# Kernel tuning notes

Hardware: AMD Instinct MI355X
Metric: run time of the kernel (lower is better)

The kernel has to match this reference:

```python
import jax, jax.numpy as jnp
import numpy as np

N = 100000   # nodes
E = 1600000  # edges
D = 64       # in_dim == hidden
H = 64       # hidden
L = 5        # GIN layers
G = 128      # graphs in batch
OUT = 10     # out_dim
BN_EPS = 1e-5


def setup_inputs() -> dict:
    key = jax.random.key(0)
    ks = jax.random.split(key, 16)
    x = jax.random.normal(ks[0], (N, D), dtype=jnp.float32)
    ei = jax.random.randint(ks[1], (2, E), 0, N, dtype=jnp.int64)
    b = jnp.sort(jax.random.randint(ks[2], (N,), 0, G, dtype=jnp.int64))
    s = 0.1
    return {
        "x": x,
        "ei": ei,
        "b": b,
        "conv_W1": jax.random.normal(ks[3], (L, D, H), dtype=jnp.float32) * s,
        "conv_b1": jnp.zeros((L, H), dtype=jnp.float32),
        "conv_W2": jax.random.normal(ks[4], (L, H, H), dtype=jnp.float32) * s,
        "conv_b2": jnp.zeros((L, H), dtype=jnp.float32),
        "bn_gamma": jnp.ones((L, H), dtype=jnp.float32),
        "bn_beta": jnp.zeros((L, H), dtype=jnp.float32),
        "head_W1": jax.random.normal(ks[5], (H, H), dtype=jnp.float32) * s,
        "head_b1": jnp.zeros((H,), dtype=jnp.float32),
        "head_W2": jax.random.normal(ks[6], (H, OUT), dtype=jnp.float32) * s,
        "head_b2": jnp.zeros((OUT,), dtype=jnp.float32),
    }


def reference(x, ei, b, conv_W1, conv_b1, conv_W2, conv_b2,
              bn_gamma, bn_beta, head_W1, head_b1, head_W2, head_b2):
    src, dst = ei[0], ei[1]
    for l in range(L):
        # GINConv (eps=0): h = x + sum_{j in N(i)} x_j  via gather + scatter-add
        agg = jax.ops.segment_sum(x[src], dst, num_segments=N)  # [N, d]
        h = x + agg
        # nn MLP: Linear -> ReLU -> Linear
        h = jax.nn.relu(h @ conv_W1[l] + conv_b1[l]) @ conv_W2[l] + conv_b2[l]
        # BatchNorm over node dim (batch statistics), then ReLU (dropout: eval)
        mean = jnp.mean(h, axis=0)
        var = jnp.var(h, axis=0)
        h = bn_gamma[l] * (h - mean) * jax.lax.rsqrt(var + BN_EPS) + bn_beta[l]
        x = jax.nn.relu(h)
    # global mean pool per graph
    sums = jax.ops.segment_sum(x, b, num_segments=G)                 # [G, H]
    cnts = jax.ops.segment_sum(jnp.ones((N,), x.dtype), b, num_segments=G)
    pooled = sums / jnp.maximum(cnts, 1.0)[:, None]
    # head: Linear -> ReLU -> (Dropout eval) -> Linear
    return jax.nn.relu(pooled @ head_W1 + head_b1) @ head_W2 + head_b2
```

## Files before the change

### kernel.cpp

```cpp
#include <hip/hip_runtime.h>

#define N_NODES 100000
#define N_EDGES 1600000
#define HDIM    64
#define NLAYERS 5
#define NGRAPH  128
#define NOUT    10
#define BN_EPS  1e-5f
#define NBUCK   196
#define EPB     8192


__global__ __launch_bounds__(256) void k_hist(const int* __restrict__ dst, int* __restrict__ counts) {
    int e = blockIdx.x * 256 + threadIdx.x;
    if (e < N_EDGES) atomicAdd(&counts[dst[e]], 1);
}

__global__ __launch_bounds__(256) void k_scan_bt(const int* __restrict__ counts, int* __restrict__ bsums) {
    __shared__ int sm[256];
    int t = threadIdx.x;
    int base = blockIdx.x * 1024 + t * 4;
    int s = 0;
#pragma unroll
    for (int k = 0; k < 4; ++k) { int i = base + k; s += (i < N_NODES) ? counts[i] : 0; }
    sm[t] = s; __syncthreads();
    for (int o = 128; o > 0; o >>= 1) { if (t < o) sm[t] += sm[t + o]; __syncthreads(); }
    if (t == 0) bsums[blockIdx.x] = sm[0];
}

__global__ void k_scan_tot(int* bsums, int nblk, int* offsets) {
    if (threadIdx.x == 0 && blockIdx.x == 0) {
        int run = 0;
        for (int i = 0; i < nblk; ++i) { int v = bsums[i]; bsums[i] = run; run += v; }
        offsets[N_NODES] = N_EDGES;
    }
}

__global__ __launch_bounds__(256) void k_scan_fin(const int* __restrict__ counts, const int* __restrict__ bsums,
                                                 int* __restrict__ offsets, int* __restrict__ cursor) {
    __shared__ int sm[256];
    int t = threadIdx.x;
    int base = blockIdx.x * 1024 + t * 4;
    int v[4]; int s = 0;
#pragma unroll
    for (int k = 0; k < 4; ++k) { int i = base + k; v[k] = (i < N_NODES) ? counts[i] : 0; s += v[k]; }
    sm[t] = s; __syncthreads();
    for (int o = 1; o < 256; o <<= 1) {
        int add = (t >= o) ? sm[t - o] : 0;
        __syncthreads();
        sm[t] += add;
        __syncthreads();
    }
    int run = bsums[blockIdx.x] + (sm[t] - s);
#pragma unroll
    for (int k = 0; k < 4; ++k) {
        int i = base + k;
        if (i < N_NODES) { offsets[i] = run; cursor[i] = run; run += v[k]; }
    }
}

__global__ void k_binit(const int* __restrict__ offs, int* __restrict__ bcursor) {
    int b = blockIdx.x * 256 + threadIdx.x;
    if (b < NBUCK) bcursor[b] = offs[b << 9];
}

__global__ __launch_bounds__(1024) void k_binfill(const int* __restrict__ src, const int* __restrict__ dst,
                                                  int* __restrict__ bcursor, unsigned* __restrict__ tmp) {
    __shared__ unsigned slots[EPB];
    __shared__ int cnt[NBUCK], lcur[NBUCK], gbase[NBUCK];
    __shared__ int lbase[NBUCK + 1];
    __shared__ int sscan[256];
    int t = threadIdx.x;
    int e0 = blockIdx.x * EPB;
    for (int i = t; i < NBUCK; i += 1024) { cnt[i] = 0; lcur[i] = 0; }
    __syncthreads();
    unsigned pk[8]; int bk[8];
#pragma unroll
    for (int k = 0; k < 8; ++k) {
        int e = e0 + k * 1024 + t;
        bk[k] = -1;
        if (e < N_EDGES) {
            int s = src[e], d = dst[e];
            int b = d >> 9;
            pk[k] = ((unsigned)(d & 511) << 17) | (unsigned)s;
            bk[k] = b;
            atomicAdd(&cnt[b], 1);
        }
    }
    __syncthreads();
    if (t < 256) sscan[t] = (t < NBUCK) ? cnt[t] : 0;
    __syncthreads();
    for (int o = 1; o < 256; o <<= 1) {
        int v = 0;
        if (t < 256 && t >= o) v = sscan[t - o];
        __syncthreads();
        if (t < 256) sscan[t] += v;
        __syncthreads();
    }
    if (t < NBUCK) {
        lbase[t] = sscan[t] - cnt[t];
        gbase[t] = atomicAdd(&bcursor[t], cnt[t]);
    }
    if (t == 0) lbase[NBUCK] = sscan[255];
    __syncthreads();
#pragma unroll
    for (int k = 0; k < 8; ++k) {
        if (bk[k] >= 0) {
            int pos = lbase[bk[k]] + atomicAdd(&lcur[bk[k]], 1);
            slots[pos] = pk[k];
        }
    }
    __syncthreads();
    int total = lbase[NBUCK];
    for (int i = t; i < total; i += 1024) {
        int lo = 0, hi = NBUCK - 1;
        while (lo < hi) { int mid = (lo + hi + 1) >> 1; if (lbase[mid] <= i) lo = mid; else hi = mid - 1; }
        tmp[gbase[lo] + (i - lbase[lo])] = slots[i];
    }
}

__global__ __launch_bounds__(1024) void k_localcsr(const unsigned* __restrict__ tmp, const int* __restrict__ offs,
                                                   int* __restrict__ cursor, int* __restrict__ csr) {
    int b = blockIdx.x;
    int nlo = b << 9;
    int nhi = nlo + 512; if (nhi > N_NODES) nhi = N_NODES;
    int base = offs[nlo], end = offs[nhi];
    for (int i = base + (int)threadIdx.x; i < end; i += 1024) {
        unsigned pk = tmp[i];
        int node = nlo + (int)(pk >> 17);
        int p = atomicAdd(&cursor[node], 1);
        csr[p] = (int)(pk & 0x1FFFFu);
    }
}


static __device__ __forceinline__ void bn_coeffs(const float* stats, const float* gam, const float* bet,
                                                 int j0, float4& sc, float4& sh) {
    const float invN = 1.0f / (float)N_NODES;
    float m, v, s;
    m = stats[j0+0]*invN; v = stats[64+j0+0]*invN - m*m; s = gam[j0+0]*rsqrtf(v+BN_EPS); sc.x = s; sh.x = bet[j0+0]-m*s;
    m = stats[j0+1]*invN; v = stats[64+j0+1]*invN - m*m; s = gam[j0+1]*rsqrtf(v+BN_EPS); sc.y = s; sh.y = bet[j0+1]-m*s;
    m = stats[j0+2]*invN; v = stats[64+j0+2]*invN - m*m; s = gam[j0+2]*rsqrtf(v+BN_EPS); sc.z = s; sh.z = bet[j0+2]-m*s;
    m = stats[j0+3]*invN; v = stats[64+j0+3]*invN - m*m; s = gam[j0+3]*rsqrtf(v+BN_EPS); sc.w = s; sh.w = bet[j0+3]-m*s;
}

static __device__ __forceinline__ float4 bn_apply(float4 v, const float4& sc, const float4& sh) {
    v.x = fmaxf(fmaf(v.x, sc.x, sh.x), 0.f);
    v.y = fmaxf(fmaf(v.y, sc.y, sh.y), 0.f);
    v.z = fmaxf(fmaf(v.z, sc.z, sh.z), 0.f);
    v.w = fmaxf(fmaf(v.w, sc.w, sh.w), 0.f);
    return v;
}

template <bool APPLY>
__global__ __launch_bounds__(256) void k_agg(const float4* __restrict__ x4, const int* __restrict__ offsets,
                                             const int* __restrict__ csr, float4* __restrict__ agg4,
                                             const float* __restrict__ stats, const float* __restrict__ gam,
                                             const float* __restrict__ bet) {
    int tid = blockIdx.x * 256 + threadIdx.x;
    int n = tid >> 4, q = tid & 15;
    if (n >= N_NODES) return;
    float4 sc, sh;
    if (APPLY) bn_coeffs(stats, gam, bet, q * 4, sc, sh);
    int beg = offsets[n], end = offsets[n + 1];
    float4 a0 = make_float4(0.f, 0.f, 0.f, 0.f);
    float4 a1 = make_float4(0.f, 0.f, 0.f, 0.f);
    int e = beg;
    for (; e + 1 < end; e += 2) {
        int s0 = csr[e], s1 = csr[e + 1];
        float4 v0 = x4[(size_t)s0 * 16 + q];
        float4 v1 = x4[(size_t)s1 * 16 + q];
        if (APPLY) { v0 = bn_apply(v0, sc, sh); v1 = bn_apply(v1, sc, sh); }
        a0.x += v0.x; a0.y += v0.y; a0.z += v0.z; a0.w += v0.w;
        a1.x += v1.x; a1.y += v1.y; a1.z += v1.z; a1.w += v1.w;
    }
    if (e < end) {
        int s0 = csr[e];
        float4 v0 = x4[(size_t)s0 * 16 + q];
        if (APPLY) v0 = bn_apply(v0, sc, sh);
        a0.x += v0.x; a0.y += v0.y; a0.z += v0.z; a0.w += v0.w;
    }
    a0.x += a1.x; a0.y += a1.y; a0.z += a1.z; a0.w += a1.w;
    agg4[(size_t)n * 16 + q] = a0;
}

#define MLP_TB 128
#define ROWS   68
template <bool APPLY>
__global__ __launch_bounds__(MLP_TB) void k_mlp2(const float* __restrict__ x, float* __restrict__ aggh2,
                                                 const float* __restrict__ W1, const float* __restrict__ b1,
                                                 const float* __restrict__ W2, const float* __restrict__ b2,
                                                 const float* __restrict__ statsPrev, const float* __restrict__ gam,
                                                 const float* __restrict__ bet, float* __restrict__ statsOut) {
    __shared__ float sm[MLP_TB * ROWS];
    __shared__ float red1[MLP_TB], red2[MLP_TB];
    int t = threadIdx.x;
    int base = blockIdx.x * MLP_TB;
    {
        int q = t & 15;
        float4 sc, sh;
        if (APPLY) bn_coeffs(statsPrev, gam, bet, q * 4, sc, sh);
        for (int i = t; i < MLP_TB * 16; i += MLP_TB) {
            int r = i >> 4;
            int n = base + r; if (n >= N_NODES) n = N_NODES - 1;
            float4 xv = ((const float4*)x)[(size_t)n * 16 + q];
            if (APPLY) xv = bn_apply(xv, sc, sh);
            float4 av = ((const float4*)aggh2)[(size_t)n * 16 + q];
            float4 s; s.x = xv.x + av.x; s.y = xv.y + av.y; s.z = xv.z + av.z; s.w = xv.w + av.w;
            *((float4*)&sm[r * ROWS + q * 4]) = s;
        }
    }
    __syncthreads();
    int n = base + t;
    bool valid = n < N_NODES;
    float* row = &sm[t * ROWS];
    float acc[64];
#pragma unroll
    for (int j = 0; j < 64; ++j) acc[j] = b1[j];
    for (int k = 0; k < 64; ++k) {
        float xk = row[k];
        const float* w = &W1[k * 64];
#pragma unroll
        for (int j = 0; j < 64; ++j) acc[j] = fmaf(xk, w[j], acc[j]);
    }
#pragma unroll
    for (int q = 0; q < 16; ++q) {
        float4 h;
        h.x = fmaxf(acc[4 * q + 0], 0.f);
        h.y = fmaxf(acc[4 * q + 1], 0.f);
        h.z = fmaxf(acc[4 * q + 2], 0.f);
        h.w = fmaxf(acc[4 * q + 3], 0.f);
        *((float4*)&row[q * 4]) = h;
    }
#pragma unroll
    for (int j = 0; j < 64; ++j) acc[j] = b2[j];
    for (int k = 0; k < 64; ++k) {
        float xk = row[k];
        const float* w = &W2[k * 64];
#pragma unroll
        for (int j = 0; j < 64; ++j) acc[j] = fmaf(xk, w[j], acc[j]);
    }
    if (valid) {
        float4* o = (float4*)(aggh2 + (size_t)n * 64);
#pragma unroll
        for (int q = 0; q < 16; ++q)
            o[q] = make_float4(acc[4 * q + 0], acc[4 * q + 1], acc[4 * q + 2], acc[4 * q + 3]);
    }
#pragma unroll
    for (int q = 0; q < 16; ++q) {
        float4 h;
        if (valid) h = make_float4(acc[4*q+0], acc[4*q+1], acc[4*q+2], acc[4*q+3]);
        else       h = make_float4(0.f, 0.f, 0.f, 0.f);
        *((float4*)&row[q * 4]) = h;
    }
    __syncthreads();
    {
        int j = t & 63, half = t >> 6;
        float s = 0.f, sq = 0.f;
        const float* col = &sm[(half * 64) * ROWS + j];
#pragma unroll 8
        for (int r = 0; r < 64; ++r) { float v = col[r * ROWS]; s += v; sq += v * v; }
        red1[t] = s; red2[t] = sq;
    }
    __syncthreads();
    if (t < 64) {
        atomicAdd(&statsOut[t], red1[t] + red1[t + 64]);
    } else {
        int j = t - 64;
        atomicAdd(&statsOut[64 + j], red2[j] + red2[j + 64]);
    }
}


__global__ void k_bounds(const int* __restrict__ b, int* __restrict__ bounds) {
    int g = threadIdx.x;
    if (g > NGRAPH) return;
    int lo = 0, hi = N_NODES;
    while (lo < hi) { int mid = (lo + hi) >> 1; if (b[mid] < g) lo = mid + 1; else hi = mid; }
    bounds[g] = lo;
}

__global__ __launch_bounds__(256) void k_pool(const float4* __restrict__ x4, const int* __restrict__ bounds,
                                              float4* __restrict__ pooled4, const float* __restrict__ stats,
                                              const float* __restrict__ gam, const float* __restrict__ bet) {
    int g = blockIdx.x;
    int beg = bounds[g], end = bounds[g + 1];
    int t = threadIdx.x;
    int q = t & 15;
    int w = t >> 4;
    float4 sc, sh;
    bn_coeffs(stats, gam, bet, q * 4, sc, sh);
    float4 a = make_float4(0.f, 0.f, 0.f, 0.f);
    for (int n = beg + w; n < end; n += 16) {
        float4 v = bn_apply(x4[(size_t)n * 16 + q], sc, sh);
        a.x += v.x; a.y += v.y; a.z += v.z; a.w += v.w;
    }
    __shared__ float4 sm[16][16];
    sm[w][q] = a; __syncthreads();
    for (int o = 8; o > 0; o >>= 1) {
        if (w < o) {
            float4 u = sm[w + o][q];
            sm[w][q].x += u.x; sm[w][q].y += u.y; sm[w][q].z += u.z; sm[w][q].w += u.w;
        }
        __syncthreads();
    }
    if (w == 0) {
        float inv = (end > beg) ? 1.0f / (float)(end - beg) : 0.0f;
        float4 r = sm[0][q];
        r.x *= inv; r.y *= inv; r.z *= inv; r.w *= inv;
        pooled4[g * 16 + q] = r;
    }
}

__global__ __launch_bounds__(128) void k_head(const float* __restrict__ pooled,
                                              const float* __restrict__ W1, const float* __restrict__ b1,
                                              const float* __restrict__ W2, const float* __restrict__ b2,
                                              float* __restrict__ out) {
    __shared__ float w1s[64 * 64];
    __shared__ float w2s[64 * NOUT];
    int t = threadIdx.x;
    for (int i = t; i < 64 * 64; i += 128) w1s[i] = W1[i];
    for (int i = t; i < 64 * NOUT; i += 128) w2s[i] = W2[i];
    __syncthreads();
    int g = t;
    float pr[64];
#pragma unroll
    for (int k = 0; k < 64; ++k) pr[k] = pooled[g * 64 + k];
    float acc[NOUT];
#pragma unroll
    for (int o = 0; o < NOUT; ++o) acc[o] = b2[o];
    for (int j = 0; j < 64; ++j) {
        float h = b1[j];
#pragma unroll
        for (int k = 0; k < 64; ++k) h = fmaf(pr[k], w1s[k * 64 + j], h);
        h = fmaxf(h, 0.f);
#pragma unroll
        for (int o = 0; o < NOUT; ++o) acc[o] = fmaf(h, w2s[j * NOUT + o], acc[o]);
    }
#pragma unroll
    for (int o = 0; o < NOUT; ++o) out[g * NOUT + o] = acc[o];
}


extern "C" void kernel_launch(void* const* d_in, const int* in_sizes, int n_in,
                              void* d_out, int out_size, void* d_ws, size_t ws_size,
                              hipStream_t stream) {
    const float* x0  = (const float*)d_in[0];
    const int*   ei  = (const int*)d_in[1];
    const int*   b   = (const int*)d_in[2];
    const float* cW1 = (const float*)d_in[3];
    const float* cb1 = (const float*)d_in[4];
    const float* cW2 = (const float*)d_in[5];
    const float* cb2 = (const float*)d_in[6];
    const float* gam = (const float*)d_in[7];
    const float* bet = (const float*)d_in[8];
    const float* hW1 = (const float*)d_in[9];
    const float* hb1 = (const float*)d_in[10];
    const float* hW2 = (const float*)d_in[11];
    const float* hb2 = (const float*)d_in[12];
    float* out = (float*)d_out;

    char* ws = (char*)d_ws;
    size_t off = 0;
    auto alloc = [&](size_t bytes) { void* p = ws + off; off += (bytes + 255) & ~(size_t)255; return p; };
    float* bufA   = (float*)alloc((size_t)N_NODES * 64 * sizeof(float));
    float* bufB   = (float*)alloc((size_t)N_NODES * 64 * sizeof(float));
    int*   csr    = (int*)alloc((size_t)N_EDGES * sizeof(int));
    int*   counts = (int*)alloc((size_t)(N_NODES + 1) * sizeof(int));
    int*   offs   = (int*)alloc((size_t)(N_NODES + 1) * sizeof(int));
    int*   cursor = (int*)alloc((size_t)(N_NODES + 1) * sizeof(int));
    int*   bsums  = (int*)alloc(256 * sizeof(int));
    int*   bcursor= (int*)alloc(256 * sizeof(int));
    float* stats  = (float*)alloc(NLAYERS * 128 * sizeof(float));
    float* pooled = (float*)alloc(NGRAPH * 64 * sizeof(float));
    int*   bounds = (int*)alloc((NGRAPH + 1) * sizeof(int));
    unsigned* tmp = (unsigned*)bufB;

    const int* src = ei;
    const int* dst = ei + N_EDGES;

    hipMemsetAsync(counts, 0, (N_NODES + 1) * sizeof(int), stream);
    hipMemsetAsync(stats, 0, NLAYERS * 128 * sizeof(float), stream);

    const int EB = (N_EDGES + 255) / 256;
    const int SB = (N_NODES + 1023) / 1024;
    const int FB = (N_EDGES + EPB - 1) / EPB;
    k_hist<<<EB, 256, 0, stream>>>(dst, counts);
    k_scan_bt<<<SB, 256, 0, stream>>>(counts, bsums);
    k_scan_tot<<<1, 1, 0, stream>>>(bsums, SB, offs);
    k_scan_fin<<<SB, 256, 0, stream>>>(counts, bsums, offs, cursor);
    k_binit<<<1, 256, 0, stream>>>(offs, bcursor);
    k_binfill<<<FB, 1024, 0, stream>>>(src, dst, bcursor, tmp);
    k_localcsr<<<NBUCK, 1024, 0, stream>>>(tmp, offs, cursor, csr);
    k_bounds<<<1, NGRAPH + 1, 0, stream>>>(b, bounds);

    const int AB = (N_NODES * 16 + 255) / 256;
    const int MB_G = (N_NODES + MLP_TB - 1) / MLP_TB;

    const float* P = x0;
    float* Q = bufA;
    float* spare = bufB;
    for (int l = 0; l < NLAYERS; ++l) {
        const float* sPrev = stats + (size_t)(l - 1) * 128;
        const float* gPrev = gam + (size_t)(l - 1) * 64;
        const float* bPrev = bet + (size_t)(l - 1) * 64;
        if (l == 0) {
            k_agg<false><<<AB, 256, 0, stream>>>((const float4*)P, offs, csr, (float4*)Q,
                                                 nullptr, nullptr, nullptr);
            k_mlp2<false><<<MB_G, MLP_TB, 0, stream>>>(P, Q,
                                                       cW1, cb1, cW2, cb2,
                                                       nullptr, nullptr, nullptr, stats);
        } else {
            k_agg<true><<<AB, 256, 0, stream>>>((const float4*)P, offs, csr, (float4*)Q,
                                                sPrev, gPrev, bPrev);
            k_mlp2<true><<<MB_G, MLP_TB, 0, stream>>>(P, Q,
                                                      cW1 + (size_t)l * 64 * 64, cb1 + l * 64,
                                                      cW2 + (size_t)l * 64 * 64, cb2 + l * 64,
                                                      sPrev, gPrev, bPrev, stats + (size_t)l * 128);
        }
        float* newSpare = (P == x0) ? spare : (float*)P;
        P = Q;
        Q = newSpare;
    }

    k_pool<<<NGRAPH, 256, 0, stream>>>((const float4*)P, bounds, (float4*)pooled,
                                       stats + 4 * 128, gam + 4 * 64, bet + 4 * 64);
    k_head<<<1, 128, 0, stream>>>(pooled, hW1, hb1, hW2, hb2, out);
}
```

Measured before the change: 830.2 us.

## Run GIN MLP on MFMA with split-bf16 (hi/lo) emulated fp32

Replaces the scalar-FMA per-node MLP kernel with a wave-per-16-node-tile kernel that uses bf16 MFMA 16x16x32 instructions. Precision is kept by a three-term hi/lo split of operands. A prologue kernel pre-converts the weights into the MFMA B-fragment layout, and the grid becomes persistent with register accumulation of the BN statistics. This trades the 64-register fp32 accumulator loop for matrix-core throughput, at the cost of extra conversion work and slightly different rounding.

```diff
diff --git a/kernel.cpp b/kernel.cpp
--- a/kernel.cpp
+++ b/kernel.cpp
@@ -9,6 +9,19 @@
 #define BN_EPS  1e-5f
 #define NBUCK   196
 #define EPB     8192
+#define NTILES  (N_NODES / 16)
+
+typedef __attribute__((ext_vector_type(8))) short bf16x8;
+typedef __attribute__((ext_vector_type(4))) float f32x4;
+
+static __device__ __forceinline__ unsigned short f2bf(float f) {
+    unsigned u = __float_as_uint(f);
+    unsigned r = (u + 0x7FFFu + ((u >> 16) & 1u)) >> 16;
+    return (unsigned short)r;
+}
+static __device__ __forceinline__ float bf2f(unsigned short h) {
+    return __uint_as_float(((unsigned)h) << 16);
+}
 
 
 __global__ __launch_bounds__(256) void k_hist(const int* __restrict__ dst, int* __restrict__ counts) {
@@ -130,6 +143,27 @@
         int node = nlo + (int)(pk >> 17);
         int p = atomicAdd(&cursor[node], 1);
         csr[p] = (int)(pk & 0x1FFFFu);
+    }
+}
+
+__global__ __launch_bounds__(256) void k_wcvt(const float* __restrict__ cW1, const float* __restrict__ cW2,
+                                              unsigned short* __restrict__ whi, unsigned short* __restrict__ wlo) {
+    int tid = blockIdx.x * 256 + threadIdx.x;
+    if (tid >= 5120) return;
+    int lane = tid & 63;
+    int r = tid >> 6;
+    int nt = r & 3;
+    int ks = (r >> 2) & 1;
+    int gemm = (r >> 3) & 1;
+    int layer = r >> 4;
+    const float* W = (gemm ? cW2 : cW1) + (size_t)layer * 4096;
+    size_t ob = ((size_t)r * 64 + lane) * 8;
+#pragma unroll
+    for (int j = 0; j < 8; ++j) {
+        float w = W[(32 * ks + 8 * (lane >> 4) + j) * 64 + 16 * nt + (lane & 15)];
+        unsigned short h = f2bf(w);
+        whi[ob + j] = h;
+        wlo[ob + j] = f2bf(w - bf2f(h));
     }
 }
 
@@ -184,90 +218,134 @@
     agg4[(size_t)n * 16 + q] = a0;
 }
 
-#define MLP_TB 128
-#define ROWS   68
 template <bool APPLY>
-__global__ __launch_bounds__(MLP_TB) void k_mlp2(const float* __restrict__ x, float* __restrict__ aggh2,
-                                                 const float* __restrict__ W1, const float* __restrict__ b1,
-                                                 const float* __restrict__ W2, const float* __restrict__ b2,
-                                                 const float* __restrict__ statsPrev, const float* __restrict__ gam,
-                                                 const float* __restrict__ bet, float* __restrict__ statsOut) {
-    __shared__ float sm[MLP_TB * ROWS];
-    __shared__ float red1[MLP_TB], red2[MLP_TB];
+__global__ __launch_bounds__(256) void k_mlp3(const float* __restrict__ x, float* __restrict__ aggh2,
+                                              const unsigned short* __restrict__ w1hi, const unsigned short* __restrict__ w1lo,
+                                              const unsigned short* __restrict__ w2hi, const unsigned short* __restrict__ w2lo,
+                                              const float* __restrict__ b1, const float* __restrict__ b2,
+                                              const float* __restrict__ statsPrev, const float* __restrict__ gam,
+                                              const float* __restrict__ bet, float* __restrict__ statsOut) {
+    __shared__ float h1s[4][16 * 68];
     int t = threadIdx.x;
-    int base = blockIdx.x * MLP_TB;
-    {
-        int q = t & 15;
-        float4 sc, sh;
-        if (APPLY) bn_coeffs(statsPrev, gam, bet, q * 4, sc, sh);
-        for (int i = t; i < MLP_TB * 16; i += MLP_TB) {
-            int r = i >> 4;
-            int n = base + r; if (n >= N_NODES) n = N_NODES - 1;
-            float4 xv = ((const float4*)x)[(size_t)n * 16 + q];
-            if (APPLY) xv = bn_apply(xv, sc, sh);
-            float4 av = ((const float4*)aggh2)[(size_t)n * 16 + q];
-            float4 s; s.x = xv.x + av.x; s.y = xv.y + av.y; s.z = xv.z + av.z; s.w = xv.w + av.w;
-            *((float4*)&sm[r * ROWS + q * 4]) = s;
-        }
-    }
-    __syncthreads();
-    int n = base + t;
-    bool valid = n < N_NODES;
-    float* row = &sm[t * ROWS];
-    float acc[64];
-#pragma unroll
-    for (int j = 0; j < 64; ++j) acc[j] = b1[j];
-    for (int k = 0; k < 64; ++k) {
-        float xk = row[k];
-        const float* w = &W1[k * 64];
-#pragma unroll
-        for (int j = 0; j < 64; ++j) acc[j] = fmaf(xk, w[j], acc[j]);
-    }
-#pragma unroll
-    for (int q = 0; q < 16; ++q) {
-        float4 h;
-        h.x = fmaxf(acc[4 * q + 0], 0.f);
-        h.y = fmaxf(acc[4 * q + 1], 0.f);
-        h.z = fmaxf(acc[4 * q + 2], 0.f);
-        h.w = fmaxf(acc[4 * q + 3], 0.f);
-        *((float4*)&row[q * 4]) = h;
-    }
-#pragma unroll
-    for (int j = 0; j < 64; ++j) acc[j] = b2[j];
-    for (int k = 0; k < 64; ++k) {
-        float xk = row[k];
-        const float* w = &W2[k * 64];
-#pragma unroll
-        for (int j = 0; j < 64; ++j) acc[j] = fmaf(xk, w[j], acc[j]);
-    }
-    if (valid) {
-        float4* o = (float4*)(aggh2 + (size_t)n * 64);
-#pragma unroll
-        for (int q = 0; q < 16; ++q)
-            o[q] = make_float4(acc[4 * q + 0], acc[4 * q + 1], acc[4 * q + 2], acc[4 * q + 3]);
-    }
-#pragma unroll
-    for (int q = 0; q < 16; ++q) {
-        float4 h;
-        if (valid) h = make_float4(acc[4*q+0], acc[4*q+1], acc[4*q+2], acc[4*q+3]);
-        else       h = make_float4(0.f, 0.f, 0.f, 0.f);
-        *((float4*)&row[q * 4]) = h;
-    }
-    __syncthreads();
-    {
-        int j = t & 63, half = t >> 6;
-        float s = 0.f, sq = 0.f;
-        const float* col = &sm[(half * 64) * ROWS + j];
-#pragma unroll 8
-        for (int r = 0; r < 64; ++r) { float v = col[r * ROWS]; s += v; sq += v * v; }
-        red1[t] = s; red2[t] = sq;
-    }
-    __syncthreads();
-    if (t < 64) {
-        atomicAdd(&statsOut[t], red1[t] + red1[t + 64]);
-    } else {
-        int j = t - 64;
-        atomicAdd(&statsOut[64 + j], red2[j] + red2[j + 64]);
+    int lane = t & 63;
+    int wv = t >> 6;
+    int lr = lane & 15;
+    int lg = lane >> 4;
+    int nw = gridDim.x * 4;
+    float* myh1 = &h1s[wv][0];
+
+    float sc[16], sh[16];
+    if (APPLY) {
+        const float invN = 1.0f / (float)N_NODES;
+#pragma unroll
+        for (int ks = 0; ks < 2; ++ks)
+#pragma unroll
+            for (int j = 0; j < 8; ++j) {
+                int f = 32 * ks + 8 * lg + j;
+                float m = statsPrev[f] * invN;
+                float v = statsPrev[64 + f] * invN - m * m;
+                float s = gam[f] * rsqrtf(v + BN_EPS);
+                sc[ks * 8 + j] = s; sh[ks * 8 + j] = bet[f] - m * s;
+            }
+    }
+    float bias1[4], bias2[4];
+#pragma unroll
+    for (int nt = 0; nt < 4; ++nt) { bias1[nt] = b1[16 * nt + lr]; bias2[nt] = b2[16 * nt + lr]; }
+
+    float st_s[4] = {0.f, 0.f, 0.f, 0.f}, st_q[4] = {0.f, 0.f, 0.f, 0.f};
+
+    for (int base = blockIdx.x * 4; base < NTILES; base += nw) {
+        int tile = base + wv;
+        bool act = tile < NTILES;
+        bf16x8 Ah[2], Al[2];
+        f32x4 acc[4];
+        if (act) {
+            int node = tile * 16 + lr;
+#pragma unroll
+            for (int ks = 0; ks < 2; ++ks) {
+                int f0 = 32 * ks + 8 * lg;
+                const float* xr = x + (size_t)node * 64 + f0;
+                const float* ar = aggh2 + (size_t)node * 64 + f0;
+                float4 xv0 = *(const float4*)xr, xv1 = *(const float4*)(xr + 4);
+                float4 av0 = *(const float4*)ar, av1 = *(const float4*)(ar + 4);
+                float in[8] = {xv0.x, xv0.y, xv0.z, xv0.w, xv1.x, xv1.y, xv1.z, xv1.w};
+                float ag[8] = {av0.x, av0.y, av0.z, av0.w, av1.x, av1.y, av1.z, av1.w};
+#pragma unroll
+                for (int j = 0; j < 8; ++j) {
+                    float v = in[j];
+                    if (APPLY) v = fmaxf(fmaf(v, sc[ks * 8 + j], sh[ks * 8 + j]), 0.f);
+                    v += ag[j];
+                    unsigned short h = f2bf(v);
+                    Ah[ks][j] = (short)h;
+                    Al[ks][j] = (short)f2bf(v - bf2f(h));
+                }
+            }
+#pragma unroll
+            for (int nt = 0; nt < 4; ++nt) {
+                f32x4 c = {bias1[nt], bias1[nt], bias1[nt], bias1[nt]};
+#pragma unroll
+                for (int ks = 0; ks < 2; ++ks) {
+                    bf16x8 bh = *(const bf16x8*)(w1hi + ((size_t)((ks * 4 + nt) * 64 + lane)) * 8);
+                    bf16x8 bl = *(const bf16x8*)(w1lo + ((size_t)((ks * 4 + nt) * 64 + lane)) * 8);
+                    c = __builtin_amdgcn_mfma_f32_16x16x32_bf16(Ah[ks], bh, c, 0, 0, 0);
+                    c = __builtin_amdgcn_mfma_f32_16x16x32_bf16(Ah[ks], bl, c, 0, 0, 0);
+                    c = __builtin_amdgcn_mfma_f32_16x16x32_bf16(Al[ks], bh, c, 0, 0, 0);
+                }
+                acc[nt] = c;
+            }
+#pragma unroll
+            for (int nt = 0; nt < 4; ++nt)
+#pragma unroll
+                for (int r = 0; r < 4; ++r)
+                    myh1[(4 * lg + r) * 68 + 16 * nt + lr] = fmaxf(acc[nt][r], 0.f);
+        }
+        __syncthreads();
+        if (act) {
+            bf16x8 A2h[2], A2l[2];
+#pragma unroll
+            for (int ks = 0; ks < 2; ++ks) {
+                const float* hr = &myh1[lr * 68 + 32 * ks + 8 * lg];
+                float4 h0 = *(const float4*)hr;
+                float4 h1v = *(const float4*)(hr + 4);
+                float hv[8] = {h0.x, h0.y, h0.z, h0.w, h1v.x, h1v.y, h1v.z, h1v.w};
+#pragma unroll
+                for (int j = 0; j < 8; ++j) {
+                    unsigned short hh = f2bf(hv[j]);
+                    A2h[ks][j] = (short)hh;
+                    A2l[ks][j] = (short)f2bf(hv[j] - bf2f(hh));
+                }
+            }
+            int nodeb = (base + wv) * 16;
+#pragma unroll
+            for (int nt = 0; nt < 4; ++nt) {
+                f32x4 c = {bias2[nt], bias2[nt], bias2[nt], bias2[nt]};
+#pragma unroll
+                for (int ks = 0; ks < 2; ++ks) {
+                    bf16x8 bh = *(const bf16x8*)(w2hi + ((size_t)((ks * 4 + nt) * 64 + lane)) * 8);
+                    bf16x8 bl = *(const bf16x8*)(w2lo + ((size_t)((ks * 4 + nt) * 64 + lane)) * 8);
+                    c = __builtin_amdgcn_mfma_f32_16x16x32_bf16(A2h[ks], bh, c, 0, 0, 0);
+                    c = __builtin_amdgcn_mfma_f32_16x16x32_bf16(A2h[ks], bl, c, 0, 0, 0);
+                    c = __builtin_amdgcn_mfma_f32_16x16x32_bf16(A2l[ks], bh, c, 0, 0, 0);
+                }
+#pragma unroll
+                for (int r = 0; r < 4; ++r) {
+                    float v = c[r];
+                    aggh2[(size_t)(nodeb + 4 * lg + r) * 64 + 16 * nt + lr] = v;
+                    st_s[nt] += v; st_q[nt] += v * v;
+                }
+            }
+        }
+        __syncthreads();
+    }
+#pragma unroll
+    for (int nt = 0; nt < 4; ++nt) {
+        float s = st_s[nt], q = st_q[nt];
+        s += __shfl_xor(s, 16); q += __shfl_xor(q, 16);
+        s += __shfl_xor(s, 32); q += __shfl_xor(q, 32);
+        if (lg == 0) {
+            atomicAdd(&statsOut[16 * nt + lr], s);
+            atomicAdd(&statsOut[64 + 16 * nt + lr], q);
+        }
     }
 }
 
@@ -374,6 +452,8 @@
     float* stats  = (float*)alloc(NLAYERS * 128 * sizeof(float));
     float* pooled = (float*)alloc(NGRAPH * 64 * sizeof(float));
     int*   bounds = (int*)alloc((NGRAPH + 1) * sizeof(int));
+    unsigned short* whi = (unsigned short*)alloc(5 * 2 * 4096 * sizeof(unsigned short));
+    unsigned short* wlo = (unsigned short*)alloc(5 * 2 * 4096 * sizeof(unsigned short));
     unsigned* tmp = (unsigned*)bufB;
 
     const int* src = ei;
@@ -393,9 +473,10 @@
     k_binfill<<<FB, 1024, 0, stream>>>(src, dst, bcursor, tmp);
     k_localcsr<<<NBUCK, 1024, 0, stream>>>(tmp, offs, cursor, csr);
     k_bounds<<<1, NGRAPH + 1, 0, stream>>>(b, bounds);
+    k_wcvt<<<20, 256, 0, stream>>>(cW1, cW2, whi, wlo);
 
     const int AB = (N_NODES * 16 + 255) / 256;
-    const int MB_G = (N_NODES + MLP_TB - 1) / MLP_TB;
+    const int MG = 782;
 
     const float* P = x0;
     float* Q = bufA;
@@ -404,19 +485,22 @@
         const float* sPrev = stats + (size_t)(l - 1) * 128;
         const float* gPrev = gam + (size_t)(l - 1) * 64;
         const float* bPrev = bet + (size_t)(l - 1) * 64;
+        const unsigned short* w1h = whi + (size_t)(l * 2) * 4096;
+        const unsigned short* w1l = wlo + (size_t)(l * 2) * 4096;
+        const unsigned short* w2h = whi + (size_t)(l * 2 + 1) * 4096;
+        const unsigned short* w2l = wlo + (size_t)(l * 2 + 1) * 4096;
         if (l == 0) {
             k_agg<false><<<AB, 256, 0, stream>>>((const float4*)P, offs, csr, (float4*)Q,
                                                  nullptr, nullptr, nullptr);
-            k_mlp2<false><<<MB_G, MLP_TB, 0, stream>>>(P, Q,
-                                                       cW1, cb1, cW2, cb2,
-                                                       nullptr, nullptr, nullptr, stats);
+            k_mlp3<false><<<MG, 256, 0, stream>>>(P, Q, w1h, w1l, w2h, w2l,
+                                                  cb1, cb2,
+                                                  nullptr, nullptr, nullptr, stats);
         } else {
             k_agg<true><<<AB, 256, 0, stream>>>((const float4*)P, offs, csr, (float4*)Q,
                                                 sPrev, gPrev, bPrev);
-            k_mlp2<true><<<MB_G, MLP_TB, 0, stream>>>(P, Q,
-                                                      cW1 + (size_t)l * 64 * 64, cb1 + l * 64,
-                                                      cW2 + (size_t)l * 64 * 64, cb2 + l * 64,
-                                                      sPrev, gPrev, bPrev, stats + (size_t)l * 128);
+            k_mlp3<true><<<MG, 256, 0, stream>>>(P, Q, w1h, w1l, w2h, w2l,
+                                                 cb1 + l * 64, cb2 + l * 64,
+                                                 sPrev, gPrev, bPrev, stats + (size_t)l * 128);
         }
         float* newSpare = (P == x0) ? spare : (float*)P;
         P = Q;
```

Result: slower. 964.0 us (+16.1%).

## Fold self-term into aggregation and split MLP matmul into column halves

Applied to the files above, without the earlier changes.

The aggregation kernel now seeds its accumulator with the node's own (BN-applied) feature, so the MLP kernel no longer reads x separately or applies the previous batch-norm. This removes one full N×64 read per layer from the MLP kernel. The MLP inner loops are also split into two 32-column halves with an un-unrolled outer loop, meant to lower instruction and register pressure, though each row element is now read from shared memory twice.

```diff
diff --git a/kernel.cpp b/kernel.cpp
--- a/kernel.cpp
+++ b/kernel.cpp
@@ -163,7 +163,8 @@
     float4 sc, sh;
     if (APPLY) bn_coeffs(stats, gam, bet, q * 4, sc, sh);
     int beg = offsets[n], end = offsets[n + 1];
-    float4 a0 = make_float4(0.f, 0.f, 0.f, 0.f);
+    float4 a0 = x4[(size_t)n * 16 + q];
+    if (APPLY) a0 = bn_apply(a0, sc, sh);
     float4 a1 = make_float4(0.f, 0.f, 0.f, 0.f);
     int e = beg;
     for (; e + 1 < end; e += 2) {
@@ -186,29 +187,19 @@
 
 #define MLP_TB 128
 #define ROWS   68
-template <bool APPLY>
-__global__ __launch_bounds__(MLP_TB) void k_mlp2(const float* __restrict__ x, float* __restrict__ aggh2,
+__global__ __launch_bounds__(MLP_TB) void k_mlp6(float* __restrict__ aggh2,
                                                  const float* __restrict__ W1, const float* __restrict__ b1,
                                                  const float* __restrict__ W2, const float* __restrict__ b2,
-                                                 const float* __restrict__ statsPrev, const float* __restrict__ gam,
-                                                 const float* __restrict__ bet, float* __restrict__ statsOut) {
+                                                 float* __restrict__ statsOut) {
     __shared__ float sm[MLP_TB * ROWS];
     __shared__ float red1[MLP_TB], red2[MLP_TB];
     int t = threadIdx.x;
     int base = blockIdx.x * MLP_TB;
-    {
-        int q = t & 15;
-        float4 sc, sh;
-        if (APPLY) bn_coeffs(statsPrev, gam, bet, q * 4, sc, sh);
-        for (int i = t; i < MLP_TB * 16; i += MLP_TB) {
-            int r = i >> 4;
-            int n = base + r; if (n >= N_NODES) n = N_NODES - 1;
-            float4 xv = ((const float4*)x)[(size_t)n * 16 + q];
-            if (APPLY) xv = bn_apply(xv, sc, sh);
-            float4 av = ((const float4*)aggh2)[(size_t)n * 16 + q];
-            float4 s; s.x = xv.x + av.x; s.y = xv.y + av.y; s.z = xv.z + av.z; s.w = xv.w + av.w;
-            *((float4*)&sm[r * ROWS + q * 4]) = s;
-        }
+    for (int i = t; i < MLP_TB * 16; i += MLP_TB) {
+        int r = i >> 4, q = i & 15;
+        int n = base + r; if (n >= N_NODES) n = N_NODES - 1;
+        float4 av = ((const float4*)aggh2)[(size_t)n * 16 + q];
+        *((float4*)&sm[r * ROWS + q * 4]) = av;
     }
     __syncthreads();
     int n = base + t;
@@ -217,11 +208,14 @@
     float acc[64];
 #pragma unroll
     for (int j = 0; j < 64; ++j) acc[j] = b1[j];
-    for (int k = 0; k < 64; ++k) {
-        float xk = row[k];
-        const float* w = &W1[k * 64];
-#pragma unroll
-        for (int j = 0; j < 64; ++j) acc[j] = fmaf(xk, w[j], acc[j]);
+#pragma unroll 1
+    for (int jh = 0; jh < 2; ++jh) {
+        for (int k = 0; k < 64; ++k) {
+            float xk = row[k];
+            const float* w = &W1[k * 64 + jh * 32];
+#pragma unroll
+            for (int j = 0; j < 32; ++j) acc[jh * 32 + j] = fmaf(xk, w[j], acc[jh * 32 + j]);
+        }
     }
 #pragma unroll
     for (int q = 0; q < 16; ++q) {
@@ -234,11 +228,14 @@
     }
 #pragma unroll
     for (int j = 0; j < 64; ++j) acc[j] = b2[j];
-    for (int k = 0; k < 64; ++k) {
-        float xk = row[k];
-        const float* w = &W2[k * 64];
-#pragma unroll
-        for (int j = 0; j < 64; ++j) acc[j] = fmaf(xk, w[j], acc[j]);
+#pragma unroll 1
+    for (int jh = 0; jh < 2; ++jh) {
+        for (int k = 0; k < 64; ++k) {
+            float xk = row[k];
+            const float* w = &W2[k * 64 + jh * 32];
+#pragma unroll
+            for (int j = 0; j < 32; ++j) acc[jh * 32 + j] = fmaf(xk, w[j], acc[jh * 32 + j]);
+        }
     }
     if (valid) {
         float4* o = (float4*)(aggh2 + (size_t)n * 64);
@@ -407,17 +404,14 @@
         if (l == 0) {
             k_agg<false><<<AB, 256, 0, stream>>>((const float4*)P, offs, csr, (float4*)Q,
                                                  nullptr, nullptr, nullptr);
-            k_mlp2<false><<<MB_G, MLP_TB, 0, stream>>>(P, Q,
-                                                       cW1, cb1, cW2, cb2,
-                                                       nullptr, nullptr, nullptr, stats);
         } else {
             k_agg<true><<<AB, 256, 0, stream>>>((const float4*)P, offs, csr, (float4*)Q,
                                                 sPrev, gPrev, bPrev);
-            k_mlp2<true><<<MB_G, MLP_TB, 0, stream>>>(P, Q,
-                                                      cW1 + (size_t)l * 64 * 64, cb1 + l * 64,
-                                                      cW2 + (size_t)l * 64 * 64, cb2 + l * 64,
-                                                      sPrev, gPrev, bPrev, stats + (size_t)l * 128);
-        }
+        }
+        k_mlp6<<<MB_G, MLP_TB, 0, stream>>>(Q,
+                                            cW1 + (size_t)l * 64 * 64, cb1 + l * 64,
+                                            cW2 + (size_t)l * 64 * 64, cb2 + l * 64,
+                                            stats + (size_t)l * 128);
         float* newSpare = (P == x0) ? spare : (float*)P;
         P = Q;
         Q = newSpare;
```

Result: slower. 941.7 us (+13.4%).
